# Performance work log

Hardware: AMD Instinct MI355X
Metric: run time of the kernel (lower is better)

The kernel has to match this reference:

```python
import jax, jax.numpy as jnp
import numpy as np

NUM_POINTS = 18
NUM_DIMS = 4
N = 8_000_000

_LAYER_DIMS = [(16, 1), (64, 16), (256, 64), (64, 256), (16, 64), (NUM_DIMS, 16)]


def setup_inputs() -> dict:
    key = jax.random.key(0)
    ks = jax.random.split(key, 13)
    inp = {"x": jax.random.uniform(ks[0], (N,), dtype=jnp.float32)}
    for i, (o, ii) in enumerate(_LAYER_DIMS):
        s = 1.0 / np.sqrt(ii)
        inp[f"W{i+1}"] = jax.random.uniform(ks[1 + 2 * i], (o, ii), dtype=jnp.float32, minval=-s, maxval=s)
        inp[f"b{i+1}"] = jax.random.uniform(ks[2 + 2 * i], (o,), dtype=jnp.float32, minval=-s, maxval=s)
    return inp


_B = jnp.array([[1.0, 0.0, 0.0], [-2.0, 2.0, 0.0], [1.0, -2.0, 1.0]], dtype=jnp.float32)


def _spline(p, d):
    # p: (3, D) control points, d: (Nb, 1) local parameter
    dd = d[:, 0]
    t = jnp.stack([jnp.ones_like(dd), dd, dd * dd], axis=-1)  # (Nb, 3)
    return (t @ _B) @ p  # (Nb, D)


def _forward(x, W1, b1, W2, b2, W3, b3, W4, b4, W5, b5, W6, b6):
    # control-point MLP on the num_points positions
    pos = jnp.arange(1, NUM_POINTS + 1, dtype=jnp.float32).reshape(NUM_POINTS, 1)
    h = jax.nn.sigmoid(pos @ W1.T + b1)
    h = jax.nn.sigmoid(h @ W2.T + b2)
    h = jax.nn.relu(h @ W3.T + b3)
    h = jax.nn.relu(h @ W4.T + b4)
    h = jax.nn.relu(h @ W5.T + b5)
    P = jnp.cumsum(h @ W6.T + b6, axis=1)  # (NUM_POINTS, NUM_DIMS)

    num_splines = NUM_POINTS - 2
    t_val = x  # (N,)

    def step(carry, xs):
        P_new, probs = carry
        i, P_next = xs
        d = ((t_val * (num_splines - 1) - i) * 0.5)[:, None]  # (N, 1)
        choice = ((d >= 0.0) & (d <= 0.5)).astype(probs.dtype)
        probs = (1.0 - choice) * probs
        P_temp = P_new
        p0 = (P_temp[0] + P_temp[2]) / 4.0 + P_temp[1] / 2.0
        p2 = P_next
        p1 = 2.0 * (P_temp[2] - (p0 + p2) / 4.0)
        P_new = jnp.stack([p0, p1, p2])
        f_prev = _spline(P_temp, d + 0.5)
        f_curr = _spline(P_new, d)
        w = jnp.cos(jnp.pi * d) ** 2 * f_prev + jnp.sin(jnp.pi * d) ** 2 * f_curr
        probs = probs + choice * w
        return (P_new, probs), None

    idx = jnp.arange(num_splines - 1, dtype=jnp.float32)
    P_nexts = P[3:NUM_POINTS]  # (num_splines-1, D)
    probs0 = jnp.zeros((t_val.shape[0], NUM_DIMS), dtype=jnp.float32)
    (_, probs), _ = jax.lax.scan(step, (P[:3], probs0), (idx, P_nexts))
    return probs


def reference(x, W1, b1, W2, b2, W3, b3, W4, b4, W5, b5, W6, b6):
    return _forward(x, W1, b1, W2, b2, W3, b3, W4, b4, W5, b5, W6, b6)
```

## Files before the change

### kernel.cpp

```cpp
#include <hip/hip_runtime.h>
#include <math.h>

#define NPTS    18
#define NDIMS   4
#define NITER   15
#define RSTRIDE 28
#define NBLK    2048
#define CHUNK   1024

__device__ __forceinline__ float sigm(float v) { return 1.0f / (1.0f + expf(-v)); }
__device__ __forceinline__ float dot4(float4 a, float4 b) {
    return fmaf(a.x, b.x, fmaf(a.y, b.y, fmaf(a.z, b.z, a.w * b.w)));
}

__global__ __launch_bounds__(512) void mlp_kernel(
    const float* __restrict__ W1, const float* __restrict__ b1,
    const float* __restrict__ W2, const float* __restrict__ b2,
    const float* __restrict__ W3, const float* __restrict__ b3,
    const float* __restrict__ W4, const float* __restrict__ b4,
    const float* __restrict__ W5, const float* __restrict__ b5,
    const float* __restrict__ W6, const float* __restrict__ b6,
    float* __restrict__ P)
{
    __shared__ float h1[16], h2[64], h3[256], h4[64], h5[16], z6[4];
    __shared__ float part[512];
    const int t = threadIdx.x;
    const float pos = (float)(blockIdx.x + 1);

    float w1r = W1[t & 15];
    float b1r = b1[t & 15];

    const int o2 = t & 63;
    float4 w2r[4];
    {
        const float4* v = (const float4*)(W2 + o2 * 16);
        #pragma unroll
        for (int k = 0; k < 4; ++k) w2r[k] = v[k];
    }
    float b2r = b2[o2];

    const int o3 = t & 255, q3 = t >> 8;
    float4 w3r[8];
    {
        const float4* v = (const float4*)(W3 + o3 * 64 + q3 * 32);
        #pragma unroll
        for (int k = 0; k < 8; ++k) w3r[k] = v[k];
    }
    float b3r = b3[o3];

    const int o4 = t & 63, q4 = t >> 6;
    float4 w4r[8];
    {
        const float4* v = (const float4*)(W4 + o4 * 256 + q4 * 32);
        #pragma unroll
        for (int k = 0; k < 8; ++k) w4r[k] = v[k];
    }
    float b4r = b4[o4];

    const int o5 = t & 15, q5 = (t >> 4) & 15;
    float4 w5r = *(const float4*)(W5 + o5 * 64 + q5 * 4);
    float b5r = b5[o5];

    const int o6 = t & 3;
    float4 w6r[4];
    {
        const float4* v = (const float4*)(W6 + o6 * 16);
        #pragma unroll
        for (int k = 0; k < 4; ++k) w6r[k] = v[k];
    }
    float b6r = b6[o6];

    if (t < 16) h1[t] = sigm(fmaf(w1r, pos, b1r));
    __syncthreads();

    if (t < 64) {
        const float4* h = (const float4*)h1;
        float a = b2r + ((dot4(w2r[0], h[0]) + dot4(w2r[1], h[1])) +
                         (dot4(w2r[2], h[2]) + dot4(w2r[3], h[3])));
        h2[t] = sigm(a);
    }
    __syncthreads();

    {
        const float4* h = (const float4*)(h2 + q3 * 32);
        float a0 = 0.f, a1 = 0.f, a2 = 0.f, a3 = 0.f;
        a0 = dot4(w3r[0], h[0]); a1 = dot4(w3r[1], h[1]);
        a2 = dot4(w3r[2], h[2]); a3 = dot4(w3r[3], h[3]);
        a0 += dot4(w3r[4], h[4]); a1 += dot4(w3r[5], h[5]);
        a2 += dot4(w3r[6], h[6]); a3 += dot4(w3r[7], h[7]);
        part[t] = (a0 + a1) + (a2 + a3);
    }
    __syncthreads();
    if (t < 256) h3[t] = fmaxf(b3r + part[t] + part[t + 256], 0.f);
    __syncthreads();

    {
        const float4* h = (const float4*)(h3 + q4 * 32);
        float a0 = 0.f, a1 = 0.f, a2 = 0.f, a3 = 0.f;
        a0 = dot4(w4r[0], h[0]); a1 = dot4(w4r[1], h[1]);
        a2 = dot4(w4r[2], h[2]); a3 = dot4(w4r[3], h[3]);
        a0 += dot4(w4r[4], h[4]); a1 += dot4(w4r[5], h[5]);
        a2 += dot4(w4r[6], h[6]); a3 += dot4(w4r[7], h[7]);
        part[t] = (a0 + a1) + (a2 + a3);
    }
    __syncthreads();
    if (t < 64) {
        float s = ((part[t] + part[t + 64]) + (part[t + 128] + part[t + 192])) +
                  ((part[t + 256] + part[t + 320]) + (part[t + 384] + part[t + 448]));
        h4[t] = fmaxf(b4r + s, 0.f);
    }
    __syncthreads();

    if (t < 256) part[t] = dot4(w5r, *(const float4*)(h4 + q5 * 4));
    __syncthreads();
    if (t < 16) {
        float s = 0.f;
        #pragma unroll
        for (int q = 0; q < 16; ++q) s += part[t + 16 * q];
        h5[t] = fmaxf(b5r + s, 0.f);
    }
    __syncthreads();

    if (t < 4) {
        const float4* h = (const float4*)h5;
        z6[t] = b6r + ((dot4(w6r[0], h[0]) + dot4(w6r[1], h[1])) +
                       (dot4(w6r[2], h[2]) + dot4(w6r[3], h[3])));
    }
    __syncthreads();

    if (t < 4) {
        float c = 0.f;
        #pragma unroll
        for (int j = 0; j <= 3; ++j) {
            float v = z6[j];
            if (j <= t) c += v;
        }
        P[blockIdx.x * NDIMS + t] = c;
    }
}

__global__ __launch_bounds__(256) void spline_kernel(
    const float* __restrict__ x, const float* __restrict__ P,
    float4* __restrict__ out4, int n)
{
    __shared__ float Praw[NPTS * NDIMS];
    __shared__ float s[NITER * RSTRIDE];
    const int t = threadIdx.x;

    if (t < NPTS * NDIMS) Praw[t] = P[t];
    __syncthreads();

    if (t < NDIMS) {
        const int j = t;
        float P0 = Praw[0 * NDIMS + j];
        float P1 = Praw[1 * NDIMS + j];
        float P2 = Praw[2 * NDIMS + j];
        #pragma unroll
        for (int i = 0; i < NITER; ++i) {
            float Pn = Praw[(3 + i) * NDIMS + j];
            float p0 = (P0 + P2) * 0.25f + P1 * 0.5f;
            float p2 = Pn;
            float p1 = 2.0f * (P2 - (p0 + p2) * 0.25f);
            float Bp = P2 - P0;
            float Cp = (P0 + P2) - 2.0f * P1;
            float Bc = 2.0f * (p1 - p0);
            float Cc = (p0 + p2) - 2.0f * p1;
            float* row = s + i * RSTRIDE;
            row[0 * 4 + j] = p0;
            row[1 * 4 + j] = Bc;
            row[2 * 4 + j] = Cc;
            row[3 * 4 + j] = Bp - Bc;
            row[4 * 4 + j] = Cp - Cc;
            P0 = p0; P1 = p1; P2 = p2;
        }
    }
    __syncthreads();

    const int gstride = NBLK * CHUNK;
    for (int base = blockIdx.x * CHUNK; base < n; base += gstride) {
        #pragma unroll
        for (int k = 0; k < 4; ++k) {
            const int i = base + k * 256 + t;
            if (i < n) {
                float u  = x[i] * 15.0f;
                float fi = floorf(u);
                fi = fminf(fmaxf(fi, 0.0f), 14.0f);
                float d  = (u - fi) * 0.5f;

                const float* row = s + (int)fi * RSTRIDE;
                float4 Ac = *(const float4*)(row + 0);
                float4 Bc = *(const float4*)(row + 4);
                float4 Cc = *(const float4*)(row + 8);
                float4 GB = *(const float4*)(row + 12);
                float4 GC = *(const float4*)(row + 16);

                float wc  = fmaf(0.5f, cospif(2.0f * d), 0.5f);
                float wcd = wc * d;

                float4 r;
                r.x = fmaf(wcd, fmaf(d, GC.x, GB.x), fmaf(d, fmaf(d, Cc.x, Bc.x), Ac.x));
                r.y = fmaf(wcd, fmaf(d, GC.y, GB.y), fmaf(d, fmaf(d, Cc.y, Bc.y), Ac.y));
                r.z = fmaf(wcd, fmaf(d, GC.z, GB.z), fmaf(d, fmaf(d, Cc.z, Bc.z), Ac.z));
                r.w = fmaf(wcd, fmaf(d, GC.w, GB.w), fmaf(d, fmaf(d, Cc.w, Bc.w), Ac.w));

                out4[i] = r;
            }
        }
    }
}

extern "C" void kernel_launch(void* const* d_in, const int* in_sizes, int n_in,
                              void* d_out, int out_size, void* d_ws, size_t ws_size,
                              hipStream_t stream)
{
    const float* x  = (const float*)d_in[0];
    const float* W1 = (const float*)d_in[1];  const float* b1 = (const float*)d_in[2];
    const float* W2 = (const float*)d_in[3];  const float* b2 = (const float*)d_in[4];
    const float* W3 = (const float*)d_in[5];  const float* b3 = (const float*)d_in[6];
    const float* W4 = (const float*)d_in[7];  const float* b4 = (const float*)d_in[8];
    const float* W5 = (const float*)d_in[9];  const float* b5 = (const float*)d_in[10];
    const float* W6 = (const float*)d_in[11]; const float* b6 = (const float*)d_in[12];

    float* P = (float*)d_ws;
    const int n = in_sizes[0];

    mlp_kernel<<<NPTS, 512, 0, stream>>>(W1, b1, W2, b2, W3, b3, W4, b4, W5, b5, W6, b6, P);

    const int blocks = min(NBLK, (n + CHUNK - 1) / CHUNK);
    spline_kernel<<<blocks, 256, 0, stream>>>(x, P, (float4*)d_out, n);
}
```

Measured before the change: 39.13 us.

## Prefetch x before table build, software-pipeline chunks, use nontemporal stores

The spline kernel now issues its x loads for the first chunk before the shared-memory coefficient table is built, so global load latency overlaps the serial table setup. The grid-stride loop is software-pipelined so the next chunk's x values load while the current chunk is evaluated. Full chunks skip per-element bounds checks, and outputs are written with nontemporal stores to avoid cache pollution. This costs more registers and adds code complexity.

```diff
diff --git a/kernel.cpp b/kernel.cpp
--- a/kernel.cpp
+++ b/kernel.cpp
@@ -7,6 +7,8 @@
 #define RSTRIDE 28
 #define NBLK    2048
 #define CHUNK   1024
+
+typedef float f32x4 __attribute__((ext_vector_type(4)));
 
 __device__ __forceinline__ float sigm(float v) { return 1.0f / (1.0f + expf(-v)); }
 __device__ __forceinline__ float dot4(float4 a, float4 b) {
@@ -139,15 +141,59 @@
     }
 }
 
+__device__ __forceinline__ f32x4 eval_one(float xc, const float* s)
+{
+    float u  = xc * 15.0f;
+    float fi = floorf(u);
+    fi = fminf(fmaxf(fi, 0.0f), 14.0f);
+    float d  = (u - fi) * 0.5f;
+
+    const float* row = s + (int)fi * RSTRIDE;
+    f32x4 Ac = *(const f32x4*)(row + 0);
+    f32x4 Bc = *(const f32x4*)(row + 4);
+    f32x4 Cc = *(const f32x4*)(row + 8);
+    f32x4 GB = *(const f32x4*)(row + 12);
+    f32x4 GC = *(const f32x4*)(row + 16);
+
+    float wc  = fmaf(0.5f, cospif(2.0f * d), 0.5f);
+    float wcd = wc * d;
+
+    f32x4 r;
+    #pragma unroll
+    for (int j = 0; j < 4; ++j)
+        r[j] = fmaf(wcd, fmaf(d, GC[j], GB[j]), fmaf(d, fmaf(d, Cc[j], Bc[j]), Ac[j]));
+    return r;
+}
+
 __global__ __launch_bounds__(256) void spline_kernel(
     const float* __restrict__ x, const float* __restrict__ P,
-    float4* __restrict__ out4, int n)
+    f32x4* __restrict__ out4, int n)
 {
     __shared__ float Praw[NPTS * NDIMS];
     __shared__ float s[NITER * RSTRIDE];
     const int t = threadIdx.x;
 
     if (t < NPTS * NDIMS) Praw[t] = P[t];
+
+    const int gstride = NBLK * CHUNK;
+    int base = blockIdx.x * CHUNK;
+    bool alive = (base < n);
+    bool cfull = false;
+    float c0 = 0.f, c1 = 0.f, c2 = 0.f, c3 = 0.f;
+    if (alive) {
+        cfull = (base + CHUNK <= n);
+        if (cfull) {
+            c0 = x[base + t];
+            c1 = x[base + 256 + t];
+            c2 = x[base + 512 + t];
+            c3 = x[base + 768 + t];
+        } else {
+            if (base + t       < n) c0 = x[base + t];
+            if (base + 256 + t < n) c1 = x[base + 256 + t];
+            if (base + 512 + t < n) c2 = x[base + 512 + t];
+            if (base + 768 + t < n) c3 = x[base + 768 + t];
+        }
+    }
     __syncthreads();
 
     if (t < NDIMS) {
@@ -176,36 +222,40 @@
     }
     __syncthreads();
 
-    const int gstride = NBLK * CHUNK;
-    for (int base = blockIdx.x * CHUNK; base < n; base += gstride) {
-        #pragma unroll
-        for (int k = 0; k < 4; ++k) {
-            const int i = base + k * 256 + t;
-            if (i < n) {
-                float u  = x[i] * 15.0f;
-                float fi = floorf(u);
-                fi = fminf(fmaxf(fi, 0.0f), 14.0f);
-                float d  = (u - fi) * 0.5f;
-
-                const float* row = s + (int)fi * RSTRIDE;
-                float4 Ac = *(const float4*)(row + 0);
-                float4 Bc = *(const float4*)(row + 4);
-                float4 Cc = *(const float4*)(row + 8);
-                float4 GB = *(const float4*)(row + 12);
-                float4 GC = *(const float4*)(row + 16);
-
-                float wc  = fmaf(0.5f, cospif(2.0f * d), 0.5f);
-                float wcd = wc * d;
-
-                float4 r;
-                r.x = fmaf(wcd, fmaf(d, GC.x, GB.x), fmaf(d, fmaf(d, Cc.x, Bc.x), Ac.x));
-                r.y = fmaf(wcd, fmaf(d, GC.y, GB.y), fmaf(d, fmaf(d, Cc.y, Bc.y), Ac.y));
-                r.z = fmaf(wcd, fmaf(d, GC.z, GB.z), fmaf(d, fmaf(d, Cc.z, Bc.z), Ac.z));
-                r.w = fmaf(wcd, fmaf(d, GC.w, GB.w), fmaf(d, fmaf(d, Cc.w, Bc.w), Ac.w));
-
-                out4[i] = r;
+    while (alive) {
+        const int nbase = base + gstride;
+        const bool nalive = (nbase < n);
+        bool nfull = false;
+        float n0 = 0.f, n1 = 0.f, n2 = 0.f, n3 = 0.f;
+        if (nalive) {
+            nfull = (nbase + CHUNK <= n);
+            if (nfull) {
+                n0 = x[nbase + t];
+                n1 = x[nbase + 256 + t];
+                n2 = x[nbase + 512 + t];
+                n3 = x[nbase + 768 + t];
+            } else {
+                if (nbase + t       < n) n0 = x[nbase + t];
+                if (nbase + 256 + t < n) n1 = x[nbase + 256 + t];
+                if (nbase + 512 + t < n) n2 = x[nbase + 512 + t];
+                if (nbase + 768 + t < n) n3 = x[nbase + 768 + t];
             }
         }
+
+        if (cfull) {
+            __builtin_nontemporal_store(eval_one(c0, s), &out4[base + t]);
+            __builtin_nontemporal_store(eval_one(c1, s), &out4[base + 256 + t]);
+            __builtin_nontemporal_store(eval_one(c2, s), &out4[base + 512 + t]);
+            __builtin_nontemporal_store(eval_one(c3, s), &out4[base + 768 + t]);
+        } else {
+            if (base + t       < n) __builtin_nontemporal_store(eval_one(c0, s), &out4[base + t]);
+            if (base + 256 + t < n) __builtin_nontemporal_store(eval_one(c1, s), &out4[base + 256 + t]);
+            if (base + 512 + t < n) __builtin_nontemporal_store(eval_one(c2, s), &out4[base + 512 + t]);
+            if (base + 768 + t < n) __builtin_nontemporal_store(eval_one(c3, s), &out4[base + 768 + t]);
+        }
+
+        base = nbase; alive = nalive; cfull = nfull;
+        c0 = n0; c1 = n1; c2 = n2; c3 = n3;
     }
 }
 
@@ -227,5 +277,5 @@
     mlp_kernel<<<NPTS, 512, 0, stream>>>(W1, b1, W2, b2, W3, b3, W4, b4, W5, b5, W6, b6, P);
 
     const int blocks = min(NBLK, (n + CHUNK - 1) / CHUNK);
-    spline_kernel<<<blocks, 256, 0, stream>>>(x, P, (float4*)d_out, n);
-}
+    spline_kernel<<<blocks, 256, 0, stream>>>(x, P, (f32x4*)d_out, n);
+}
```

Measured after the change: 36.41 us. -7.0%, faster.
